# Kernel optimization log

Hardware: AMD Instinct MI355X
Metric: run time of the kernel (lower is better)

Reference implementation:

```python
import jax, jax.numpy as jnp
import numpy as np
from jax import lax

N = 50000
E = 320000
IN_DIM = 128
OUT_DIM = 64
N_CHANNEL = 8
KERNEL = 3
N_REL = 500
BN_EPS = 1e-5


def setup_inputs() -> dict:
    key = jax.random.key(0)
    ks = jax.random.split(key, 10)
    inp = jax.random.normal(ks[0], (N, IN_DIM), dtype=jnp.float32)
    heads = jax.random.randint(ks[1], (E,), 0, N)
    rels = jax.random.randint(ks[2], (E,), 0, N_REL)
    tails = jax.random.randint(ks[3], (E,), 0, N)
    triple = jnp.stack([heads, rels, tails], axis=1).astype(jnp.int64)
    # parameters
    limit_W = float(np.sqrt(6.0 / (IN_DIM + OUT_DIM)))  # xavier_uniform
    W = jax.random.uniform(ks[4], (IN_DIM, OUT_DIM), minval=-limit_W, maxval=limit_W, dtype=jnp.float32)
    rel_embed = jax.random.normal(ks[5], (N_REL, OUT_DIM), dtype=jnp.float32)
    fan_in = 1 * KERNEL * KERNEL
    b = float(1.0 / np.sqrt(fan_in))
    conv_w = jax.random.uniform(ks[6], (N_CHANNEL, 1, KERNEL, KERNEL), minval=-b, maxval=b, dtype=jnp.float32)
    conv_b = jax.random.uniform(ks[7], (N_CHANNEL,), minval=-b, maxval=b, dtype=jnp.float32)
    fc_in = N_CHANNEL * (OUT_DIM - KERNEL + 1) * (3 - KERNEL + 1)
    bf = float(1.0 / np.sqrt(fc_in))
    fc_w = jax.random.uniform(ks[8], (1, fc_in), minval=-bf, maxval=bf, dtype=jnp.float32)
    bn1_gamma = jnp.ones((1,), jnp.float32)
    bn1_beta = jnp.zeros((1,), jnp.float32)
    bn2_gamma = jnp.ones((N_CHANNEL,), jnp.float32)
    bn2_beta = jnp.zeros((N_CHANNEL,), jnp.float32)
    return {"input": inp, "triple": triple, "W": W, "rel_embed": rel_embed,
            "conv_w": conv_w, "conv_b": conv_b, "fc_w": fc_w,
            "bn1_gamma": bn1_gamma, "bn1_beta": bn1_beta,
            "bn2_gamma": bn2_gamma, "bn2_beta": bn2_beta}


def _bn_eval(x, gamma, beta):
    # eval-mode BatchNorm with running_mean=0, running_var=1
    scale = gamma / jnp.sqrt(1.0 + BN_EPS)
    return x * scale.reshape(1, -1, 1, 1) + beta.reshape(1, -1, 1, 1)


def reference(input, triple, W, rel_embed, conv_w, conv_b, fc_w,
              bn1_gamma, bn1_beta, bn2_gamma, bn2_beta):
    n = input.shape[0]
    inp = input @ W                       # [N, out_dim]
    head = triple[:, 0]
    tail = triple[:, 2]
    h = inp[head]                         # [E, D]
    r = rel_embed[triple[:, 1]]           # [E, D]
    t = inp[tail]                         # [E, D]
    # energy function: [E,1,D,3] -> bn1 -> conv -> bn2 -> relu -> fc
    x = jnp.stack([h, r, t], axis=-1)[:, None, :, :]   # [E,1,D,3]
    x = _bn_eval(x, bn1_gamma, bn1_beta)
    y = lax.conv_general_dilated(x, conv_w, (1, 1), 'VALID',
                                 dimension_numbers=('NCHW', 'OIHW', 'NCHW'))
    y = y + conv_b.reshape(1, -1, 1, 1)                 # [E,C,D-2,1]
    y = jax.nn.relu(_bn_eval(y, bn2_gamma, bn2_beta))
    y = y.reshape(y.shape[0], -1)
    e = y @ fc_w[0]                                     # [E]
    e = jax.nn.leaky_relu(e, 0.01)
    # sparse softmax over rows (head) then sparse mm with input_
    m = jax.ops.segment_max(e, head, num_segments=n)
    ex = jnp.exp(e - m[head])
    denom = jax.ops.segment_sum(ex, head, num_segments=n)
    attn = ex / denom[head]
    agg = jax.ops.segment_sum(attn[:, None] * t, head, num_segments=n)
    return jax.nn.elu(agg + inp)
```

## Files before the change

kernel.cpp:

```cpp
#include <hip/hip_runtime.h>
#include <hip/hip_bf16.h>
#include <stdint.h>

#define IN_DIM   128
#define OUT_DIM  64
#define NCH      8
#define N_REL    500
#define BN_EPS   1e-5f
#define CAP      32


#define KEEP(x) asm volatile("" : "+v"(x))

__device__ __forceinline__ float dpp_shl1(float x) {
    return __int_as_float(__builtin_amdgcn_update_dpp(
        0, __float_as_int(x), 0x130, 0xf, 0xf, true));
}

__device__ __forceinline__ float sget(float x) {
    return __int_as_float(__builtin_amdgcn_readfirstlane(__float_as_int(x)));
}

__device__ __forceinline__ void fold_cw_thread(
    const float* __restrict__ conv_w, const float* __restrict__ conv_b,
    const float* __restrict__ bn1g, const float* __restrict__ bn1b,
    const float* __restrict__ bn2g, const float* __restrict__ bn2b,
    float* __restrict__ cw, int c)
{
    if (c >= NCH) return;
    float rs  = rsqrtf(1.f + BN_EPS);
    float s1  = bn1g[0] * rs;
    float be1 = bn1b[0];
    float s2  = bn2g[c] * rs;
    float k1  = s1 * s2;
    float wsum = 0.f;
    for (int d = 0; d < 3; ++d) {
        float a  = conv_w[c * 9 + d * 3 + 0];
        float b  = conv_w[c * 9 + d * 3 + 1];
        float cc = conv_w[c * 9 + d * 3 + 2];
        wsum += a + b + cc;
        cw[c * 3 + d]      = k1 * a;
        cw[24 + c * 3 + d] = k1 * b;
        cw[48 + c * 3 + d] = k1 * cc;
    }
    cw[72 + c] = (be1 * wsum + conv_b[c]) * s2 + bn2b[c];
}

__global__ __launch_bounds__(256) void k_build(
    const float* __restrict__ X, const float* __restrict__ W,
    const int* __restrict__ triple, const float* __restrict__ rel_embed,
    const float* __restrict__ conv_w, const float* __restrict__ conv_b,
    const float* __restrict__ bn1g, const float* __restrict__ bn1b,
    const float* __restrict__ bn2g, const float* __restrict__ bn2b,
    float* __restrict__ inp, int* __restrict__ cnt, int2* __restrict__ rt32,
    float* __restrict__ cw, float* __restrict__ Rt,
    int E, int N, int ngemm, int nbucket)
{
    __shared__ float Wl[IN_DIM * OUT_DIM];
    __shared__ float Xl[32 * IN_DIM];

    if ((int)blockIdx.x < ngemm) {
        const int rows0 = blockIdx.x * 32;
        const float4* W4 = (const float4*)W;
        for (int i = threadIdx.x; i < IN_DIM * OUT_DIM / 4; i += 256)
            ((float4*)Wl)[i] = W4[i];
        for (int i = threadIdx.x; i < 32 * IN_DIM / 4; i += 256) {
            int r = i >> 5, k4 = i & 31;
            int rr = rows0 + r;
            float4 v = make_float4(0.f, 0.f, 0.f, 0.f);
            if (rr < N) v = ((const float4*)X)[(unsigned)rr * (IN_DIM / 4) + k4];
            ((float4*)Xl)[i] = v;
        }
        __syncthreads();

        const int w = threadIdx.x >> 6;
        const int c = threadIdx.x & 63;
        float acc[8];
        #pragma unroll
        for (int r = 0; r < 8; ++r) acc[r] = 0.f;

        for (int k4 = 0; k4 < IN_DIM / 4; ++k4) {
            int k = k4 * 4;
            float w0 = Wl[(k + 0) * OUT_DIM + c];
            float w1 = Wl[(k + 1) * OUT_DIM + c];
            float w2 = Wl[(k + 2) * OUT_DIM + c];
            float w3 = Wl[(k + 3) * OUT_DIM + c];
            #pragma unroll
            for (int r = 0; r < 8; ++r) {
                const float4 x = *(const float4*)&Xl[(w * 8 + r) * IN_DIM + k];
                acc[r] = fmaf(x.w, w3, fmaf(x.z, w2, fmaf(x.y, w1, fmaf(x.x, w0, acc[r]))));
            }
        }
        #pragma unroll
        for (int r = 0; r < 8; ++r) {
            int rr = rows0 + w * 8 + r;
            if (rr < N) inp[(unsigned)rr * OUT_DIM + c] = acc[r];
        }
    } else if ((int)blockIdx.x < ngemm + nbucket) {
        const int bb   = blockIdx.x - ngemm;
        const int gtid = bb * 256 + threadIdx.x;
        if (bb == 0 && threadIdx.x < NCH)
            fold_cw_thread(conv_w, conv_b, bn1g, bn1b, bn2g, bn2b, cw, threadIdx.x);
        if (gtid < E) {
            int j = gtid;
            int h = triple[3 * j], r = triple[3 * j + 1], t = triple[3 * j + 2];
            h = min(max(h, 0), N - 1);
            r = min(max(r, 0), N_REL - 1);
            t = min(max(t, 0), N - 1);
            int pos = atomicAdd(&cnt[h], 1);
            if (pos < CAP) rt32[(unsigned)h * CAP + pos] = make_int2(r, t);
        }
    } else {
        const int rb  = blockIdx.x - ngemm - nbucket;
        const int ln  = threadIdx.x & 63;
        const int rel = rb * 4 + (threadIdx.x >> 6);
        if (rel < N_REL) {
            float rr = rel_embed[(unsigned)rel * OUT_DIM + ln];
            float r1 = dpp_shl1(rr), r2 = dpp_shl1(r1);
            float rs = rsqrtf(1.f + BN_EPS);
            float s1 = bn1g[0] * rs;
            float q[NCH];
            #pragma unroll
            for (int c = 0; c < NCH; ++c) {
                float k1 = s1 * (bn2g[c] * rs);
                float b0 = k1 * conv_w[c * 9 + 1];
                float b1 = k1 * conv_w[c * 9 + 4];
                float b2 = k1 * conv_w[c * 9 + 7];
                q[c] = fmaf(b0, rr, fmaf(b1, r1, b2 * r2));
            }
            float4* dst = (float4*)&Rt[(unsigned)rel * (OUT_DIM * NCH) + ln * NCH];
            dst[0] = make_float4(q[0], q[1], q[2], q[3]);
            dst[1] = make_float4(q[4], q[5], q[6], q[7]);
        }
    }
}

__device__ __forceinline__ float dpp_wave_sum(float x) {
    x += __int_as_float(__builtin_amdgcn_update_dpp(0, __float_as_int(x), 0x111, 0xf, 0xf, true));
    x += __int_as_float(__builtin_amdgcn_update_dpp(0, __float_as_int(x), 0x112, 0xf, 0xf, true));
    x += __int_as_float(__builtin_amdgcn_update_dpp(0, __float_as_int(x), 0x114, 0xf, 0xf, true));
    x += __int_as_float(__builtin_amdgcn_update_dpp(0, __float_as_int(x), 0x118, 0xf, 0xf, true));
    x += __int_as_float(__builtin_amdgcn_update_dpp(0, __float_as_int(x), 0x142, 0xf, 0xf, true));
    x += __int_as_float(__builtin_amdgcn_update_dpp(0, __float_as_int(x), 0x143, 0xf, 0xf, true));
    return __int_as_float(__builtin_amdgcn_readlane(__float_as_int(x), 63));
}

__global__ __launch_bounds__(256) void k_fused_all(
    const float* __restrict__ inp, const float* __restrict__ Rt,
    const float* __restrict__ cw, const float* __restrict__ fc_w,
    const int* __restrict__ cnt, const int2* __restrict__ rt32,
    float* __restrict__ out, int N)
{
    const int lane   = threadIdx.x & 63;
    const int wave   = (blockIdx.x * (blockDim.x >> 6)) + (threadIdx.x >> 6);
    const int nwaves = gridDim.x * (blockDim.x >> 6);

    float cA0[NCH], cA1[NCH], cA2[NCH], cC0[NCH], cC1[NCH], cC2[NCH], k0c[NCH];
    #pragma unroll
    for (int c = 0; c < NCH; ++c) {
        cA0[c] = sget(cw[c * 3 + 0]);
        cA1[c] = sget(cw[c * 3 + 1]);
        cA2[c] = sget(cw[c * 3 + 2]);
        cC0[c] = sget(cw[48 + c * 3 + 0]);
        cC1[c] = sget(cw[48 + c * 3 + 1]);
        cC2[c] = sget(cw[48 + c * 3 + 2]);
        k0c[c] = sget(cw[72 + c]);
    }

    float fcl[NCH];
    #pragma unroll
    for (int c = 0; c < NCH; ++c) {
        fcl[c] = (lane < 62) ? fc_w[c * 62 + lane] : 0.f;
        KEEP(fcl[c]);
    }

    for (int h = wave; h < N; h += nwaves) {
        const int deg = min(cnt[h], CAP);

        float h0 = inp[(unsigned)h * OUT_DIM + lane];
        float h1 = dpp_shl1(h0);
        float h2 = dpp_shl1(h1);
        float Ht[NCH];
        #pragma unroll
        for (int c = 0; c < NCH; ++c) {
            float v = k0c[c];
            v = fmaf(cA0[c], h0, v);
            v = fmaf(cA1[c], h1, v);
            v = fmaf(cA2[c], h2, v);
            Ht[c] = v;
            KEEP(Ht[c]);
        }

        float m_run = -INFINITY, l_run = 0.f, agg = 0.f;
        int2 rtv = make_int2(0, 0);
        if (lane < deg) rtv = rt32[(unsigned)h * CAP + lane];

        if (deg > 0) {
#define LOADQ(KK, Q0, Q1)                                                       \
            {   int rkL = __builtin_amdgcn_readlane(rtv.x, (KK));               \
                const float4* qp = (const float4*)&Rt[(unsigned)rkL * (OUT_DIM * NCH) \
                                                      + (unsigned)(lane * NCH)]; \
                Q0 = qp[0]; Q1 = qp[1]; }
#define LOADT(KK, TT)                                                           \
            {   int tkL = __builtin_amdgcn_readlane(rtv.y, (KK));               \
                TT = inp[(unsigned)tkL * OUT_DIM + lane]; }

#define CHB(c, QC, T0, T1, T2, AX)                                              \
                { float y = Ht[c] + (QC);                                       \
                  y = fmaf(cC0[c], (T0), y);                                    \
                  y = fmaf(cC1[c], (T1), y);                                    \
                  y = fmaf(cC2[c], (T2), y);                                    \
                  AX = fmaf(fmaxf(y, 0.f), fcl[c], AX); }

#define CH8(Q0, Q1, T0, T1, T2, X0, X1)                                         \
                CHB(0, (Q0).x, T0, T1, T2, X0) CHB(1, (Q0).y, T0, T1, T2, X1)   \
                CHB(2, (Q0).z, T0, T1, T2, X0) CHB(3, (Q0).w, T0, T1, T2, X1)   \
                CHB(4, (Q1).x, T0, T1, T2, X0) CHB(5, (Q1).y, T0, T1, T2, X1)   \
                CHB(6, (Q1).z, T0, T1, T2, X0) CHB(7, (Q1).w, T0, T1, T2, X1)

#define SMUPD(S, TT)                                                            \
            {   float ev = fmaxf((S), 0.01f * (S));                             \
                bool  up = ev > m_run;                                          \
                float d  = up ? (m_run - ev) : (ev - m_run);                    \
                float e  = __expf(d);                                           \
                float sc = up ? e : 1.f;                                        \
                float wk = up ? 1.f : e;                                        \
                agg   = fmaf(agg, sc, wk * (TT));                               \
                l_run = fmaf(l_run, sc, wk);                                    \
                m_run = fmaxf(m_run, ev); }

            float4 qa0, qa1, qb0, qb1;
            float  tta, ttb;
            LOADQ(0, qa0, qa1) LOADT(0, tta)
            LOADQ(1, qb0, qb1) LOADT(1, ttb)

            int k = 0;
            for (; k + 1 < deg; k += 2) {
                float t1a = dpp_shl1(tta), t2a = dpp_shl1(t1a);
                float t1b = dpp_shl1(ttb), t2b = dpp_shl1(t1b);
                float aA0 = 0.f, aA1 = 0.f, aB0 = 0.f, aB1 = 0.f;
                CH8(qa0, qa1, tta, t1a, t2a, aA0, aA1)
                CH8(qb0, qb1, ttb, t1b, t2b, aB0, aB1)

                float4 nqa0, nqa1, nqb0, nqb1;
                float  nta, ntb;
                LOADQ(k + 2, nqa0, nqa1) LOADT(k + 2, nta)
                LOADQ(k + 3, nqb0, nqb1) LOADT(k + 3, ntb)

                float sA = dpp_wave_sum(aA0 + aA1);
                float sB = dpp_wave_sum(aB0 + aB1);

                SMUPD(sA, tta)
                SMUPD(sB, ttb)

                qa0 = nqa0; qa1 = nqa1; qb0 = nqb0; qb1 = nqb1;
                tta = nta;  ttb = ntb;
            }
            if (k < deg) {
                float t1a = dpp_shl1(tta), t2a = dpp_shl1(t1a);
                float aA0 = 0.f, aA1 = 0.f;
                CH8(qa0, qa1, tta, t1a, t2a, aA0, aA1)
                float sA = dpp_wave_sum(aA0 + aA1);
                SMUPD(sA, tta)
            }
#undef SMUPD
#undef CH8
#undef CHB
#undef LOADT
#undef LOADQ
        }
        float aggn = (l_run > 0.f) ? agg / l_run : 0.f;
        float x = aggn + h0;
        float y = x > 0.f ? x : (__expf(x) - 1.f);
        out[(unsigned)h * OUT_DIM + lane] = y;
    }
}

extern "C" void kernel_launch(void* const* d_in, const int* in_sizes, int n_in,
                              void* d_out, int out_size, void* d_ws, size_t ws_size,
                              hipStream_t stream)
{
    const float* input     = (const float*)d_in[0];
    const int*   triple    = (const int*)d_in[1];
    const float* W         = (const float*)d_in[2];
    const float* rel_embed = (const float*)d_in[3];
    const float* conv_w    = (const float*)d_in[4];
    const float* conv_b    = (const float*)d_in[5];
    const float* fc_w      = (const float*)d_in[6];
    const float* bn1g      = (const float*)d_in[7];
    const float* bn1b      = (const float*)d_in[8];
    const float* bn2g      = (const float*)d_in[9];
    const float* bn2b      = (const float*)d_in[10];
    float*       out       = (float*)d_out;

    const int N = in_sizes[0] / IN_DIM;
    const int E = in_sizes[1] / 3;

    auto align = [](size_t x) { return (x + 255) & ~(size_t)255; };
    char* base = (char*)d_ws;
    size_t o = 0;
    float* inp  = (float*)(base + o); o = align(o + (size_t)N * OUT_DIM * 4);
    int2*  rt32 = (int2*)(base + o);  o = align(o + (size_t)N * CAP * 8);
    float* cw   = (float*)(base + o); o = align(o + 80 * 4);
    int*   cnt  = (int*)(base + o);   o = align(o + (size_t)N * 4);
    float* Rt   = (float*)(base + o); o = align(o + (size_t)N_REL * OUT_DIM * NCH * 4);

    hipMemsetAsync(cnt, 0, (size_t)N * 4, stream);

    const int ngemm   = (N + 31) / 32;
    const int nbucket = (E + 255) / 256;
    const int ntab    = (N_REL + 3) / 4;
    k_build<<<ngemm + nbucket + ntab, 256, 0, stream>>>(
        input, W, triple, rel_embed, conv_w, conv_b, bn1g, bn1b, bn2g, bn2b,
        inp, cnt, rt32, cw, Rt, E, N, ngemm, nbucket);

    const int nblk = (N + 3) / 4;
    k_fused_all<<<nblk, 256, 0, stream>>>(inp, Rt, cw, fc_w,
                                          cnt, rt32, out, N);
}
```

Measured before the change: 184.7 us.

## Use 4x4 register-tiled GEMM with transposed swizzled X tile in shared memory

The input projection GEMM now computes a 4x4 output micro-tile per thread over a 64-row block. The X tile is stored transposed with an XOR swizzle so each thread can read float4 values along rows. This cuts shared-memory loads per FMA and halves the number of GEMM blocks. In exchange, shared memory per block grows (At is 32KB on top of the 32KB Wl), which may lower occupancy for the other block roles in the same launch.

```diff
diff --git a/kernel.cpp b/kernel.cpp
--- a/kernel.cpp
+++ b/kernel.cpp
@@ -57,44 +57,57 @@
     int E, int N, int ngemm, int nbucket)
 {
     __shared__ float Wl[IN_DIM * OUT_DIM];
-    __shared__ float Xl[32 * IN_DIM];
+    __shared__ float At[64 * IN_DIM];
 
     if ((int)blockIdx.x < ngemm) {
-        const int rows0 = blockIdx.x * 32;
+        const int rows0 = blockIdx.x * 64;
         const float4* W4 = (const float4*)W;
         for (int i = threadIdx.x; i < IN_DIM * OUT_DIM / 4; i += 256)
             ((float4*)Wl)[i] = W4[i];
-        for (int i = threadIdx.x; i < 32 * IN_DIM / 4; i += 256) {
-            int r = i >> 5, k4 = i & 31;
+        for (int i = threadIdx.x; i < 64 * IN_DIM / 4; i += 256) {
+            int r  = i >> 5;
+            int k4 = i & 31;
             int rr = rows0 + r;
             float4 v = make_float4(0.f, 0.f, 0.f, 0.f);
             if (rr < N) v = ((const float4*)X)[(unsigned)rr * (IN_DIM / 4) + k4];
-            ((float4*)Xl)[i] = v;
+            int rsw = r ^ ((k4 & 7) << 2);
+            At[(k4 * 4 + 0) * 64 + rsw] = v.x;
+            At[(k4 * 4 + 1) * 64 + rsw] = v.y;
+            At[(k4 * 4 + 2) * 64 + rsw] = v.z;
+            At[(k4 * 4 + 3) * 64 + rsw] = v.w;
         }
         __syncthreads();
 
-        const int w = threadIdx.x >> 6;
-        const int c = threadIdx.x & 63;
-        float acc[8];
-        #pragma unroll
-        for (int r = 0; r < 8; ++r) acc[r] = 0.f;
-
-        for (int k4 = 0; k4 < IN_DIM / 4; ++k4) {
-            int k = k4 * 4;
-            float w0 = Wl[(k + 0) * OUT_DIM + c];
-            float w1 = Wl[(k + 1) * OUT_DIM + c];
-            float w2 = Wl[(k + 2) * OUT_DIM + c];
-            float w3 = Wl[(k + 3) * OUT_DIM + c];
-            #pragma unroll
-            for (int r = 0; r < 8; ++r) {
-                const float4 x = *(const float4*)&Xl[(w * 8 + r) * IN_DIM + k];
-                acc[r] = fmaf(x.w, w3, fmaf(x.z, w2, fmaf(x.y, w1, fmaf(x.x, w0, acc[r]))));
-            }
-        }
-        #pragma unroll
-        for (int r = 0; r < 8; ++r) {
-            int rr = rows0 + w * 8 + r;
-            if (rr < N) inp[(unsigned)rr * OUT_DIM + c] = acc[r];
+        const int tx = threadIdx.x & 15;
+        const int ty = threadIdx.x >> 4;
+        float a00=0.f,a01=0.f,a02=0.f,a03=0.f;
+        float a10=0.f,a11=0.f,a12=0.f,a13=0.f;
+        float a20=0.f,a21=0.f,a22=0.f,a23=0.f;
+        float a30=0.f,a31=0.f,a32=0.f,a33=0.f;
+
+        #pragma unroll 8
+        for (int k = 0; k < IN_DIM; ++k) {
+            const float4 a = *(const float4*)&At[k * 64 + ((ty * 4) ^ (((k >> 2) & 7) << 2))];
+            const float4 b = *(const float4*)&Wl[k * 64 + tx * 4];
+            a00 = fmaf(a.x, b.x, a00); a01 = fmaf(a.x, b.y, a01);
+            a02 = fmaf(a.x, b.z, a02); a03 = fmaf(a.x, b.w, a03);
+            a10 = fmaf(a.y, b.x, a10); a11 = fmaf(a.y, b.y, a11);
+            a12 = fmaf(a.y, b.z, a12); a13 = fmaf(a.y, b.w, a13);
+            a20 = fmaf(a.z, b.x, a20); a21 = fmaf(a.z, b.y, a21);
+            a22 = fmaf(a.z, b.z, a22); a23 = fmaf(a.z, b.w, a23);
+            a30 = fmaf(a.w, b.x, a30); a31 = fmaf(a.w, b.y, a31);
+            a32 = fmaf(a.w, b.z, a32); a33 = fmaf(a.w, b.w, a33);
+        }
+
+        {
+            int rr = rows0 + ty * 4 + 0;
+            if (rr < N) *(float4*)&inp[(unsigned)rr * OUT_DIM + tx * 4] = make_float4(a00, a01, a02, a03);
+            rr = rows0 + ty * 4 + 1;
+            if (rr < N) *(float4*)&inp[(unsigned)rr * OUT_DIM + tx * 4] = make_float4(a10, a11, a12, a13);
+            rr = rows0 + ty * 4 + 2;
+            if (rr < N) *(float4*)&inp[(unsigned)rr * OUT_DIM + tx * 4] = make_float4(a20, a21, a22, a23);
+            rr = rows0 + ty * 4 + 3;
+            if (rr < N) *(float4*)&inp[(unsigned)rr * OUT_DIM + tx * 4] = make_float4(a30, a31, a32, a33);
         }
     } else if ((int)blockIdx.x < ngemm + nbucket) {
         const int bb   = blockIdx.x - ngemm;
@@ -307,7 +320,7 @@
 
     hipMemsetAsync(cnt, 0, (size_t)N * 4, stream);
 
-    const int ngemm   = (N + 31) / 32;
+    const int ngemm   = (N + 63) / 64;
     const int nbucket = (E + 255) / 256;
     const int ntab    = (N_REL + 3) / 4;
     k_build<<<ngemm + nbucket + ntab, 256, 0, stream>>>(
```

After: 174.2 us. 1.06x faster.

## Replace LDS-staged GEMM with register-tiled 4x4 direct-global-load GEMM

Applied to the files above, without the earlier changes.

The input@W GEMM in the build kernel no longer stages W and X tiles in shared memory. Each thread now computes a 4-row by 4-column register tile, loading float4 rows of X and W straight from global memory (through L1/L2), and each block covers 64 rows instead of 32. This removes the 48KB of LDS and the block barrier, which should raise occupancy and let the GEMM blocks overlap better with the bucketing and table blocks in the same launch. In exchange, reuse now depends on the caches instead of LDS, and every thread re-reads W from global memory.

```diff
diff --git a/kernel.cpp b/kernel.cpp
--- a/kernel.cpp
+++ b/kernel.cpp
@@ -56,46 +56,52 @@
     float* __restrict__ cw, float* __restrict__ Rt,
     int E, int N, int ngemm, int nbucket)
 {
-    __shared__ float Wl[IN_DIM * OUT_DIM];
-    __shared__ float Xl[32 * IN_DIM];
-
     if ((int)blockIdx.x < ngemm) {
-        const int rows0 = blockIdx.x * 32;
+        const int rows0 = blockIdx.x * 64;
+        const int tx = threadIdx.x & 15;
+        const int ty = threadIdx.x >> 4;
+        const int r0 = rows0 + ty * 4;
+        const float4* X4 = (const float4*)X;
         const float4* W4 = (const float4*)W;
-        for (int i = threadIdx.x; i < IN_DIM * OUT_DIM / 4; i += 256)
-            ((float4*)Wl)[i] = W4[i];
-        for (int i = threadIdx.x; i < 32 * IN_DIM / 4; i += 256) {
-            int r = i >> 5, k4 = i & 31;
-            int rr = rows0 + r;
-            float4 v = make_float4(0.f, 0.f, 0.f, 0.f);
-            if (rr < N) v = ((const float4*)X)[(unsigned)rr * (IN_DIM / 4) + k4];
-            ((float4*)Xl)[i] = v;
-        }
-        __syncthreads();
-
-        const int w = threadIdx.x >> 6;
-        const int c = threadIdx.x & 63;
-        float acc[8];
-        #pragma unroll
-        for (int r = 0; r < 8; ++r) acc[r] = 0.f;
-
+        const unsigned rA = (unsigned)min(r0 + 0, N - 1);
+        const unsigned rB = (unsigned)min(r0 + 1, N - 1);
+        const unsigned rC = (unsigned)min(r0 + 2, N - 1);
+        const unsigned rD = (unsigned)min(r0 + 3, N - 1);
+
+        float4 c0 = make_float4(0.f, 0.f, 0.f, 0.f);
+        float4 c1 = c0, c2 = c0, c3 = c0;
+
+#define GSTEP(XC, BV)                                                           \
+        c0.x = fmaf(xa.XC, BV.x, c0.x); c0.y = fmaf(xa.XC, BV.y, c0.y);         \
+        c0.z = fmaf(xa.XC, BV.z, c0.z); c0.w = fmaf(xa.XC, BV.w, c0.w);         \
+        c1.x = fmaf(xb.XC, BV.x, c1.x); c1.y = fmaf(xb.XC, BV.y, c1.y);         \
+        c1.z = fmaf(xb.XC, BV.z, c1.z); c1.w = fmaf(xb.XC, BV.w, c1.w);         \
+        c2.x = fmaf(xc.XC, BV.x, c2.x); c2.y = fmaf(xc.XC, BV.y, c2.y);         \
+        c2.z = fmaf(xc.XC, BV.z, c2.z); c2.w = fmaf(xc.XC, BV.w, c2.w);         \
+        c3.x = fmaf(xd.XC, BV.x, c3.x); c3.y = fmaf(xd.XC, BV.y, c3.y);         \
+        c3.z = fmaf(xd.XC, BV.z, c3.z); c3.w = fmaf(xd.XC, BV.w, c3.w);
+
+        #pragma unroll 2
         for (int k4 = 0; k4 < IN_DIM / 4; ++k4) {
-            int k = k4 * 4;
-            float w0 = Wl[(k + 0) * OUT_DIM + c];
-            float w1 = Wl[(k + 1) * OUT_DIM + c];
-            float w2 = Wl[(k + 2) * OUT_DIM + c];
-            float w3 = Wl[(k + 3) * OUT_DIM + c];
-            #pragma unroll
-            for (int r = 0; r < 8; ++r) {
-                const float4 x = *(const float4*)&Xl[(w * 8 + r) * IN_DIM + k];
-                acc[r] = fmaf(x.w, w3, fmaf(x.z, w2, fmaf(x.y, w1, fmaf(x.x, w0, acc[r]))));
-            }
-        }
-        #pragma unroll
-        for (int r = 0; r < 8; ++r) {
-            int rr = rows0 + w * 8 + r;
-            if (rr < N) inp[(unsigned)rr * OUT_DIM + c] = acc[r];
-        }
+            const float4 xa = X4[rA * (IN_DIM / 4) + k4];
+            const float4 xb = X4[rB * (IN_DIM / 4) + k4];
+            const float4 xc = X4[rC * (IN_DIM / 4) + k4];
+            const float4 xd = X4[rD * (IN_DIM / 4) + k4];
+            const float4 b0 = W4[(k4 * 4 + 0) * 16 + tx];
+            const float4 b1 = W4[(k4 * 4 + 1) * 16 + tx];
+            const float4 b2 = W4[(k4 * 4 + 2) * 16 + tx];
+            const float4 b3 = W4[(k4 * 4 + 3) * 16 + tx];
+            GSTEP(x, b0)
+            GSTEP(y, b1)
+            GSTEP(z, b2)
+            GSTEP(w, b3)
+        }
+#undef GSTEP
+
+        if (r0 + 0 < N) *(float4*)&inp[(unsigned)(r0 + 0) * OUT_DIM + tx * 4] = c0;
+        if (r0 + 1 < N) *(float4*)&inp[(unsigned)(r0 + 1) * OUT_DIM + tx * 4] = c1;
+        if (r0 + 2 < N) *(float4*)&inp[(unsigned)(r0 + 2) * OUT_DIM + tx * 4] = c2;
+        if (r0 + 3 < N) *(float4*)&inp[(unsigned)(r0 + 3) * OUT_DIM + tx * 4] = c3;
     } else if ((int)blockIdx.x < ngemm + nbucket) {
         const int bb   = blockIdx.x - ngemm;
         const int gtid = bb * 256 + threadIdx.x;
@@ -307,7 +313,7 @@
 
     hipMemsetAsync(cnt, 0, (size_t)N * 4, stream);
 
-    const int ngemm   = (N + 31) / 32;
+    const int ngemm   = (N + 63) / 64;
     const int nbucket = (E + 255) / 256;
     const int ntab    = (N_REL + 3) / 4;
     k_build<<<ngemm + nbucket + ntab, 256, 0, stream>>>(
```

After: 190.5 us. +3.1%, slower.
